# Optimization experiments

Hardware: AMD Instinct MI355X
Metric: run time of the kernel (lower is better)

## Reference

```python
import jax, jax.numpy as jnp
import numpy as np

B, S, D, H = 2, 2048, 1024, 16
HEAD_DIM = D // H  # 64


def setup_inputs() -> dict:
    key = jax.random.key(0)
    ks = jax.random.split(key, 7)
    x = jax.random.normal(ks[0], (B, S, D), dtype=jnp.float32)
    W_q = jax.random.normal(ks[1], (D, D), dtype=jnp.float32) * 0.02
    W_k = jax.random.normal(ks[2], (D, D), dtype=jnp.float32) * 0.02
    W_v = jax.random.normal(ks[3], (D, D), dtype=jnp.float32) * 0.02
    W_o = jax.random.normal(ks[4], (D, D), dtype=jnp.float32) * 0.02 / np.sqrt(2 * 12)
    b_o = jnp.zeros((D,), dtype=jnp.float32)
    # Ragged prefix attention_mask: per-row valid lengths in [S/2, S];
    # row 0 forced to full length so max_valid_len == S statically (jit-safe).
    lengths = jax.random.randint(ks[5], (B,), S // 2, S + 1)
    lengths = lengths.at[0].set(S)
    attention_mask = (jnp.arange(S)[None, :] < lengths[:, None]).astype(jnp.float32)
    return {"x": x, "attention_mask": attention_mask, "W_q": W_q, "W_k": W_k,
            "W_v": W_v, "W_o": W_o, "b_o": b_o}


def reference(x, attention_mask, W_q, W_k, W_v, W_o, b_o):
    b, s, d = x.shape
    h, hd = H, HEAD_DIM
    # QKV projections (no bias, qkv_bias=False)
    q = (x @ W_q.T).reshape(b, s, h, hd).transpose(0, 2, 1, 3)  # [b,h,s,hd]
    # Masking keys/values at invalid (padded) positions; for prefix masks this
    # is exactly the module's per-batch packing loop (max_valid_len == s).
    m = attention_mask[:, None, :, None]  # [b,1,s,1]
    k = ((x @ W_k.T).reshape(b, s, h, hd).transpose(0, 2, 1, 3)) * m
    v = ((x @ W_v.T).reshape(b, s, h, hd).transpose(0, 2, 1, 3)) * m
    # Naive causal attention, same op order as the torch module:
    # mask with -inf first, then scale by 1/sqrt(head_dim), then softmax.
    causal = jnp.triu(jnp.ones((s, s), dtype=bool), 1)  # True above diagonal
    scores = jnp.einsum('bhqd,bhkd->bhqk', q, k)
    scores = jnp.where(causal[None, None], -jnp.inf, scores)
    att = jax.nn.softmax(scores / jnp.sqrt(jnp.float32(hd)), axis=-1)
    ctx = jnp.einsum('bhqk,bhkd->bhqd', att, v)  # [b,h,s,hd]
    ctx = ctx.transpose(0, 2, 1, 3).reshape(b, s, d)
    # Output projection (dropout is inference no-op)
    return ctx @ W_o.T + b_o
```

## Files before the change

### kernel.cpp

```cpp
#include <hip/hip_runtime.h>

#define B_  2
#define S_  2048
#define D_  1024
#define H_  16
#define HD_ 64
#define N3_ 3072
#define M_  4096

typedef _Float16 f16;
typedef _Float16 f16x4 __attribute__((ext_vector_type(4)));
typedef _Float16 f16x8 __attribute__((ext_vector_type(8)));
typedef float    f32x4 __attribute__((ext_vector_type(4)));

__device__ __forceinline__ void async16(const f16* g, f16* l) {
  __builtin_amdgcn_global_load_lds(
      (const __attribute__((address_space(1))) unsigned int*)g,
      (__attribute__((address_space(3))) unsigned int*)l, 16, 0, 0);
}

__global__ __launch_bounds__(256)
void cvt_f32_f16(const float* __restrict__ src, f16* __restrict__ dst,
                 int n4, float scale) {
  int i = blockIdx.x * 256 + threadIdx.x;
  if (i >= n4) return;
  float4 v = ((const float4*)src)[i];
  f16x4 o = { (f16)(v.x * scale), (f16)(v.y * scale),
              (f16)(v.z * scale), (f16)(v.w * scale) };
  ((f16x4*)dst)[i] = o;
}

template<int QKV>
__global__ __launch_bounds__(256)
void gemm_nt(const f16* __restrict__ A, const f16* __restrict__ Bw,
             f16* __restrict__ Cq, float* __restrict__ Cf,
             const float* __restrict__ mask, const float* __restrict__ bias,
             int Ndim, int Kdim) {
  __shared__ f16 As[128 * 32];
  __shared__ f16 Bs[128 * 32];

  const int tid  = threadIdx.x;
  const int lane = tid & 63;
  const int w    = tid >> 6;
  const int lcol = lane & 15;
  const int quad = lane >> 4;
  const int wave_m = w >> 1, wave_n = w & 1;

  const int m0 = blockIdx.y * 128;
  const int n0 = blockIdx.x * 128;

  const int c  = (lane & 3) ^ ((lane >> 3) & 3);
  const int rr = lane >> 2;
  const int u0 = 2 * w, u1 = 2 * w + 1;
  const f16* gA0 = A  + (size_t)(m0 + u0 * 16 + rr) * Kdim + c * 8;
  const f16* gA1 = A  + (size_t)(m0 + u1 * 16 + rr) * Kdim + c * 8;
  const f16* gB0 = Bw + (size_t)(n0 + u0 * 16 + rr) * Kdim + c * 8;
  const f16* gB1 = Bw + (size_t)(n0 + u1 * 16 + rr) * Kdim + c * 8;
  f16* lA0 = As + u0 * 512;
  f16* lA1 = As + u1 * 512;
  f16* lB0 = Bs + u0 * 512;
  f16* lB1 = Bs + u1 * 512;

  int offA[4], offB[4];
#pragma unroll
  for (int i = 0; i < 4; i++) {
    int ra = wave_m * 64 + i * 16 + lcol;
    offA[i] = ra * 32 + ((quad ^ ((ra >> 1) & 3)) * 8);
    int rb = wave_n * 64 + i * 16 + lcol;
    offB[i] = rb * 32 + ((quad ^ ((rb >> 1) & 3)) * 8);
  }

  const f32x4 zero = {0.f, 0.f, 0.f, 0.f};
  f32x4 acc[4][4];
#pragma unroll
  for (int i = 0; i < 4; i++)
#pragma unroll
    for (int j = 0; j < 4; j++) acc[i][j] = zero;

  for (int k0 = 0; k0 < Kdim; k0 += 32) {
    __syncthreads();
    async16(gA0 + k0, lA0);
    async16(gA1 + k0, lA1);
    async16(gB0 + k0, lB0);
    async16(gB1 + k0, lB1);
    __syncthreads();

    f16x8 af[4], bf[4];
#pragma unroll
    for (int i = 0; i < 4; i++) af[i] = *(const f16x8*)(As + offA[i]);
#pragma unroll
    for (int i = 0; i < 4; i++) bf[i] = *(const f16x8*)(Bs + offB[i]);
#pragma unroll
    for (int mi = 0; mi < 4; mi++)
#pragma unroll
      for (int ni = 0; ni < 4; ni++)
        acc[mi][ni] = __builtin_amdgcn_mfma_f32_16x16x32_f16(
            af[mi], bf[ni], acc[mi][ni], 0, 0, 0);
  }

#pragma unroll
  for (int mi = 0; mi < 4; mi++) {
#pragma unroll
    for (int r = 0; r < 4; r++) {
      int mg = m0 + wave_m * 64 + mi * 16 + quad * 4 + r;
      float mk = QKV ? mask[mg] : 0.f;
#pragma unroll
      for (int ni = 0; ni < 4; ni++) {
        int ng = n0 + wave_n * 64 + ni * 16 + lcol;
        float v = acc[mi][ni][r];
        if (QKV) {
          if (ng >= D_) v *= mk;
          Cq[(size_t)mg * Ndim + ng] = (f16)v;
        } else {
          Cf[(size_t)mg * Ndim + ng] = v + bias[ng];
        }
      }
    }
  }
}

__global__ __launch_bounds__(256)
void transpose_v(const f16* __restrict__ qkv, f16* __restrict__ vt) {
  __shared__ f16 t[64][72];
  const int tid = threadIdx.x;
  const int bh  = blockIdx.y;
  const int b   = bh >> 4, h = bh & 15;
  const int s0  = blockIdx.x * 64;
  {
    const int hdc = (tid & 15) * 4;
    const int sl  = tid >> 4;
#pragma unroll
    for (int i = 0; i < 4; i++) {
      int s = sl + i * 16;
      f16x4 v = *(const f16x4*)(qkv + (size_t)(b * S_ + s0 + s) * N3_ +
                                2 * D_ + h * HD_ + hdc);
      *(f16x4*)&t[s][hdc] = v;
    }
  }
  __syncthreads();
  {
    const int sc4 = (tid & 15) * 4;
    const int hd  = tid >> 4;
#pragma unroll
    for (int i = 0; i < 4; i++) {
      int hh = hd + i * 16;
      f16x4 v = { t[sc4][hh], t[sc4 + 1][hh], t[sc4 + 2][hh], t[sc4 + 3][hh] };
      *(f16x4*)(vt + (size_t)(bh * HD_ + hh) * S_ + s0 + sc4) = v;
    }
  }
}

__global__ __launch_bounds__(256)
void flash_attn2(const f16* __restrict__ qkv, const f16* __restrict__ vt,
                 f16* __restrict__ ctx) {
  __shared__ f16 Ks[64 * 64];
  __shared__ f16 Vs[64 * 64];

  const int tid  = threadIdx.x;
  const int lane = tid & 63;
  const int w    = tid >> 6;
  const int lcol = lane & 15;
  const int quad = lane >> 4;
  const int lx   = lcol & 7;
  const int bh   = blockIdx.y;
  const int b    = bh >> 4, h = bh & 15;
  const int pair = blockIdx.x;

  const int rsub = lane >> 3;
  const int gch  = (lane & 7) ^ rsub;
  const int krow0 = w * 8 + rsub;
  const int krow1 = 32 + w * 8 + rsub;
  const f16* Kg = qkv + (size_t)b * S_ * N3_ + D_ + h * HD_;
  const f16* Vg = vt + (size_t)bh * HD_ * S_;
  f16* ldsK0 = Ks + (w * 8) * 64;
  f16* ldsK1 = Ks + (32 + w * 8) * 64;
  f16* ldsV0 = Vs + (w * 8) * 64;
  f16* ldsV1 = Vs + (32 + w * 8) * 64;

  const f32x4 zero = {0.f, 0.f, 0.f, 0.f};

  for (int phase = 0; phase < 2; phase++) {
    const int qt   = phase ? (31 - pair) : pair;
    const int qrow = qt * 64 + w * 16 + lcol;
    const f16* Qp = qkv + (size_t)(b * S_ + qrow) * N3_ + h * HD_;
    const f16x8 qb0 = *(const f16x8*)(Qp + quad * 8);
    const f16x8 qb1 = *(const f16x8*)(Qp + 32 + quad * 8);

    f32x4 o[4];
#pragma unroll
    for (int i = 0; i < 4; i++) o[i] = zero;
    float mx = -1e30f, lp = 0.f;

    for (int kt = 0; kt <= qt; kt++) {
      const int kbase = kt * 64;
      __syncthreads();
      async16(Kg + (size_t)(kbase + krow0) * N3_ + gch * 8, ldsK0);
      async16(Kg + (size_t)(kbase + krow1) * N3_ + gch * 8, ldsK1);
      async16(Vg + (size_t)krow0 * S_ + kbase + gch * 8, ldsV0);
      async16(Vg + (size_t)krow1 * S_ + kbase + gch * 8, ldsV1);
      __syncthreads();

      f32x4 sc[4];
#pragma unroll
      for (int ct = 0; ct < 4; ct++) {
        const f16* kr = Ks + (ct * 16 + lcol) * 64;
        f16x8 k0 = *(const f16x8*)(kr + ((quad    ) ^ lx) * 8);
        f16x8 k1 = *(const f16x8*)(kr + ((quad + 4) ^ lx) * 8);
        f32x4 z = zero;
        z = __builtin_amdgcn_mfma_f32_16x16x32_f16(k0, qb0, z, 0, 0, 0);
        z = __builtin_amdgcn_mfma_f32_16x16x32_f16(k1, qb1, z, 0, 0, 0);
        sc[ct] = z;
      }
      if (kt == qt) {
#pragma unroll
        for (int ct = 0; ct < 4; ct++) {
          int koff = ct * 16 + quad * 4;
          int qoff = w * 16 + lcol;
#pragma unroll
          for (int r = 0; r < 4; r++)
            if (koff + r > qoff) sc[ct][r] = -1e30f;
        }
      }
      float t = sc[0][0];
#pragma unroll
      for (int ct = 0; ct < 4; ct++)
#pragma unroll
        for (int r = 0; r < 4; r++) t = fmaxf(t, sc[ct][r]);
      t = fmaxf(t, __shfl_xor(t, 16));
      t = fmaxf(t, __shfl_xor(t, 32));
      const float nm = fmaxf(mx, t);
      const float alpha = exp2f(mx - nm);
      mx = nm;
      lp *= alpha;
#pragma unroll
      for (int ht = 0; ht < 4; ht++) {
#pragma unroll
        for (int r = 0; r < 4; r++) o[ht][r] *= alpha;
      }
      f16x4 pf[4];
#pragma unroll
      for (int ct = 0; ct < 4; ct++) {
        float e0 = exp2f(sc[ct][0] - nm);
        float e1 = exp2f(sc[ct][1] - nm);
        float e2 = exp2f(sc[ct][2] - nm);
        float e3 = exp2f(sc[ct][3] - nm);
        lp += (e0 + e1) + (e2 + e3);
        f16x4 p = { (f16)e0, (f16)e1, (f16)e2, (f16)e3 };
        pf[ct] = p;
      }
#pragma unroll
      for (int ht = 0; ht < 4; ht++) {
        const f16* vr = Vs + (ht * 16 + lcol) * 64 + (quad & 1) * 4;
#pragma unroll
        for (int ct = 0; ct < 4; ct++) {
          f16x4 vf = *(const f16x4*)(vr + (((2 * ct + (quad >> 1)) ^ lx) * 8));
          o[ht] = __builtin_amdgcn_mfma_f32_16x16x16f16(vf, pf[ct], o[ht], 0, 0, 0);
        }
      }
    }

    lp += __shfl_xor(lp, 16);
    lp += __shfl_xor(lp, 32);
    const float inv = 1.f / lp;
    f16* cp = ctx + (size_t)(b * S_ + qrow) * D_ + h * HD_ + quad * 4;
#pragma unroll
    for (int ht = 0; ht < 4; ht++) {
      f16x4 ov = { (f16)(o[ht][0] * inv), (f16)(o[ht][1] * inv),
                   (f16)(o[ht][2] * inv), (f16)(o[ht][3] * inv) };
      *(f16x4*)(cp + ht * 16) = ov;
    }
  }
}

extern "C" void kernel_launch(void* const* d_in, const int* in_sizes, int n_in,
                              void* d_out, int out_size, void* d_ws, size_t ws_size,
                              hipStream_t stream) {
  (void)in_sizes; (void)n_in; (void)out_size; (void)ws_size;
  const float* x  = (const float*)d_in[0];
  const float* am = (const float*)d_in[1];
  const float* Wq = (const float*)d_in[2];
  const float* Wk = (const float*)d_in[3];
  const float* Wv = (const float*)d_in[4];
  const float* Wo = (const float*)d_in[5];
  const float* bo = (const float*)d_in[6];
  float* out = (float*)d_out;

  f16* ws   = (f16*)d_ws;
  f16* wqkv = ws;
  f16* wo16 = wqkv + (size_t)3 * D_ * D_;
  f16* xb   = wo16 + (size_t)D_ * D_;
  f16* qkvb = xb + (size_t)M_ * D_;
  f16* vtb  = qkvb + (size_t)M_ * N3_;
  f16* ctxb = vtb + (size_t)M_ * D_;

  const float qscale = 0.125f * 1.4426950408889634f;

  cvt_f32_f16<<<dim3(M_ * D_ / 1024), 256, 0, stream>>>(x, xb, M_ * D_ / 4, 1.0f);
  cvt_f32_f16<<<dim3(D_ * D_ / 1024), 256, 0, stream>>>(Wq, wqkv, D_ * D_ / 4, qscale);
  cvt_f32_f16<<<dim3(D_ * D_ / 1024), 256, 0, stream>>>(Wk, wqkv + (size_t)D_ * D_, D_ * D_ / 4, 1.0f);
  cvt_f32_f16<<<dim3(D_ * D_ / 1024), 256, 0, stream>>>(Wv, wqkv + (size_t)2 * D_ * D_, D_ * D_ / 4, 1.0f);
  cvt_f32_f16<<<dim3(D_ * D_ / 1024), 256, 0, stream>>>(Wo, wo16, D_ * D_ / 4, 1.0f);

  gemm_nt<1><<<dim3(N3_ / 128, M_ / 128), 256, 0, stream>>>(
      xb, wqkv, qkvb, nullptr, am, nullptr, N3_, D_);
  transpose_v<<<dim3(S_ / 64, B_ * H_), 256, 0, stream>>>(qkvb, vtb);
  flash_attn2<<<dim3(16, B_ * H_), 256, 0, stream>>>(qkvb, vtb, ctxb);
  gemm_nt<0><<<dim3(D_ / 128, M_ / 128), 256, 0, stream>>>(
      ctxb, wo16, nullptr, out, nullptr, bo, D_, D_);
}
```

Baseline: 214.4 us.

## Share K/V tiles across paired query tiles, widen GEMM K-step, fuse weight casts

The flash attention kernel now walks both query tiles of a causal pair in one pass over keys, so each K/V tile is loaded once and reused for both. Previously the two tiles were processed one after the other, each reloading K/V. The block index is also remapped to a flat 1D grid that interleaves heads. Separately, the GEMM's K tile grows from 32 to 64 with a new XOR swizzle, halving the number of barrier pairs, and the four weight conversion launches are merged into one 2D launch. Costs are more registers for two accumulator sets and doubled LDS in the GEMM, which may lower occupancy.

```diff
diff --git a/kernel.cpp b/kernel.cpp
--- a/kernel.cpp
+++ b/kernel.cpp
@@ -30,44 +30,62 @@
   ((f16x4*)dst)[i] = o;
 }
 
+__global__ __launch_bounds__(256)
+void cvt_weights(const float* __restrict__ Wq, const float* __restrict__ Wk,
+                 const float* __restrict__ Wv, const float* __restrict__ Wo,
+                 f16* __restrict__ dst, float qscale) {
+  const int m = blockIdx.y;
+  const float* src = (m == 0) ? Wq : (m == 1) ? Wk : (m == 2) ? Wv : Wo;
+  const float scale = (m == 0) ? qscale : 1.0f;
+  int i = blockIdx.x * 256 + threadIdx.x;
+  float4 v = ((const float4*)src)[i];
+  f16x4 o = { (f16)(v.x * scale), (f16)(v.y * scale),
+              (f16)(v.z * scale), (f16)(v.w * scale) };
+  ((f16x4*)(dst + (size_t)m * D_ * D_))[i] = o;
+}
+
 template<int QKV>
 __global__ __launch_bounds__(256)
 void gemm_nt(const f16* __restrict__ A, const f16* __restrict__ Bw,
              f16* __restrict__ Cq, float* __restrict__ Cf,
              const float* __restrict__ mask, const float* __restrict__ bias,
              int Ndim, int Kdim) {
-  __shared__ f16 As[128 * 32];
-  __shared__ f16 Bs[128 * 32];
+  __shared__ f16 As[128 * 64];
+  __shared__ f16 Bs[128 * 64];
 
   const int tid  = threadIdx.x;
   const int lane = tid & 63;
   const int w    = tid >> 6;
   const int lcol = lane & 15;
   const int quad = lane >> 4;
+  const int lx   = lcol & 7;
   const int wave_m = w >> 1, wave_n = w & 1;
 
   const int m0 = blockIdx.y * 128;
   const int n0 = blockIdx.x * 128;
 
-  const int c  = (lane & 3) ^ ((lane >> 3) & 3);
-  const int rr = lane >> 2;
-  const int u0 = 2 * w, u1 = 2 * w + 1;
-  const f16* gA0 = A  + (size_t)(m0 + u0 * 16 + rr) * Kdim + c * 8;
-  const f16* gA1 = A  + (size_t)(m0 + u1 * 16 + rr) * Kdim + c * 8;
-  const f16* gB0 = Bw + (size_t)(n0 + u0 * 16 + rr) * Kdim + c * 8;
-  const f16* gB1 = Bw + (size_t)(n0 + u1 * 16 + rr) * Kdim + c * 8;
-  f16* lA0 = As + u0 * 512;
-  f16* lA1 = As + u1 * 512;
-  f16* lB0 = Bs + u0 * 512;
-  f16* lB1 = Bs + u1 * 512;
+  const int rr  = lane >> 3;
+  const int gch = (lane & 7) ^ rr;
+
+  const f16* gA[4];
+  const f16* gB[4];
+  f16* lA[4];
+  f16* lB[4];
+#pragma unroll
+  for (int i = 0; i < 4; i++) {
+    int seg = i * 4 + w;
+    int row = seg * 8 + rr;
+    gA[i] = A  + (size_t)(m0 + row) * Kdim + gch * 8;
+    gB[i] = Bw + (size_t)(n0 + row) * Kdim + gch * 8;
+    lA[i] = As + seg * 512;
+    lB[i] = Bs + seg * 512;
+  }
 
   int offA[4], offB[4];
 #pragma unroll
   for (int i = 0; i < 4; i++) {
-    int ra = wave_m * 64 + i * 16 + lcol;
-    offA[i] = ra * 32 + ((quad ^ ((ra >> 1) & 3)) * 8);
-    int rb = wave_n * 64 + i * 16 + lcol;
-    offB[i] = rb * 32 + ((quad ^ ((rb >> 1) & 3)) * 8);
+    offA[i] = (wave_m * 64 + i * 16 + lcol) * 64;
+    offB[i] = (wave_n * 64 + i * 16 + lcol) * 64;
   }
 
   const f32x4 zero = {0.f, 0.f, 0.f, 0.f};
@@ -77,25 +95,29 @@
 #pragma unroll
     for (int j = 0; j < 4; j++) acc[i][j] = zero;
 
-  for (int k0 = 0; k0 < Kdim; k0 += 32) {
+  for (int k0 = 0; k0 < Kdim; k0 += 64) {
     __syncthreads();
-    async16(gA0 + k0, lA0);
-    async16(gA1 + k0, lA1);
-    async16(gB0 + k0, lB0);
-    async16(gB1 + k0, lB1);
+#pragma unroll
+    for (int i = 0; i < 4; i++) async16(gA[i] + k0, lA[i]);
+#pragma unroll
+    for (int i = 0; i < 4; i++) async16(gB[i] + k0, lB[i]);
     __syncthreads();
 
-    f16x8 af[4], bf[4];
-#pragma unroll
-    for (int i = 0; i < 4; i++) af[i] = *(const f16x8*)(As + offA[i]);
-#pragma unroll
-    for (int i = 0; i < 4; i++) bf[i] = *(const f16x8*)(Bs + offB[i]);
-#pragma unroll
-    for (int mi = 0; mi < 4; mi++)
-#pragma unroll
-      for (int ni = 0; ni < 4; ni++)
-        acc[mi][ni] = __builtin_amdgcn_mfma_f32_16x16x32_f16(
-            af[mi], bf[ni], acc[mi][ni], 0, 0, 0);
+#pragma unroll
+    for (int ks = 0; ks < 2; ks++) {
+      const int co = ((quad + 4 * ks) ^ lx) * 8;
+      f16x8 af[4], bf[4];
+#pragma unroll
+      for (int i = 0; i < 4; i++) af[i] = *(const f16x8*)(As + offA[i] + co);
+#pragma unroll
+      for (int i = 0; i < 4; i++) bf[i] = *(const f16x8*)(Bs + offB[i] + co);
+#pragma unroll
+      for (int mi = 0; mi < 4; mi++)
+#pragma unroll
+        for (int ni = 0; ni < 4; ni++)
+          acc[mi][ni] = __builtin_amdgcn_mfma_f32_16x16x32_f16(
+              af[mi], bf[ni], acc[mi][ni], 0, 0, 0);
+    }
   }
 
 #pragma unroll
@@ -151,7 +173,7 @@
 }
 
 __global__ __launch_bounds__(256)
-void flash_attn2(const f16* __restrict__ qkv, const f16* __restrict__ vt,
+void flash_attn3(const f16* __restrict__ qkv, const f16* __restrict__ vt,
                  f16* __restrict__ ctx) {
   __shared__ f16 Ks[64 * 64];
   __shared__ f16 Vs[64 * 64];
@@ -162,9 +184,13 @@
   const int lcol = lane & 15;
   const int quad = lane >> 4;
   const int lx   = lcol & 7;
-  const int bh   = blockIdx.y;
+
+  const int id   = blockIdx.x;
+  const int bh   = (id & 7) + 8 * ((id >> 3) & 3);
+  const int pair = id >> 5;
   const int b    = bh >> 4, h = bh & 15;
-  const int pair = blockIdx.x;
+  const int qtA  = 31 - pair;
+  const int qtB  = pair;
 
   const int rsub = lane >> 3;
   const int gch  = (lane & 7) ^ rsub;
@@ -179,96 +205,110 @@
 
   const f32x4 zero = {0.f, 0.f, 0.f, 0.f};
 
-  for (int phase = 0; phase < 2; phase++) {
-    const int qt   = phase ? (31 - pair) : pair;
-    const int qrow = qt * 64 + w * 16 + lcol;
-    const f16* Qp = qkv + (size_t)(b * S_ + qrow) * N3_ + h * HD_;
-    const f16x8 qb0 = *(const f16x8*)(Qp + quad * 8);
-    const f16x8 qb1 = *(const f16x8*)(Qp + 32 + quad * 8);
-
-    f32x4 o[4];
-#pragma unroll
-    for (int i = 0; i < 4; i++) o[i] = zero;
-    float mx = -1e30f, lp = 0.f;
-
-    for (int kt = 0; kt <= qt; kt++) {
-      const int kbase = kt * 64;
-      __syncthreads();
-      async16(Kg + (size_t)(kbase + krow0) * N3_ + gch * 8, ldsK0);
-      async16(Kg + (size_t)(kbase + krow1) * N3_ + gch * 8, ldsK1);
-      async16(Vg + (size_t)krow0 * S_ + kbase + gch * 8, ldsV0);
-      async16(Vg + (size_t)krow1 * S_ + kbase + gch * 8, ldsV1);
-      __syncthreads();
-
-      f32x4 sc[4];
+  const int qrowA = qtA * 64 + w * 16 + lcol;
+  const int qrowB = qtB * 64 + w * 16 + lcol;
+  const f16* QpA = qkv + (size_t)(b * S_ + qrowA) * N3_ + h * HD_;
+  const f16* QpB = qkv + (size_t)(b * S_ + qrowB) * N3_ + h * HD_;
+  const f16x8 qbA0 = *(const f16x8*)(QpA + quad * 8);
+  const f16x8 qbA1 = *(const f16x8*)(QpA + 32 + quad * 8);
+  const f16x8 qbB0 = *(const f16x8*)(QpB + quad * 8);
+  const f16x8 qbB1 = *(const f16x8*)(QpB + 32 + quad * 8);
+
+  f32x4 oA[4], oB[4];
+  float mxA = -1e30f, lpA = 0.f, mxB = -1e30f, lpB = 0.f;
+#pragma unroll
+  for (int i = 0; i < 4; i++) { oA[i] = zero; oB[i] = zero; }
+
+  auto process = [&](int qt, const f16x8& qb0, const f16x8& qb1,
+                     f32x4* o, float& mx, float& lp, int kt) {
+    f32x4 sc[4];
+#pragma unroll
+    for (int ct = 0; ct < 4; ct++) {
+      const f16* kr = Ks + (ct * 16 + lcol) * 64;
+      f16x8 k0 = *(const f16x8*)(kr + ((quad    ) ^ lx) * 8);
+      f16x8 k1 = *(const f16x8*)(kr + ((quad + 4) ^ lx) * 8);
+      f32x4 z = zero;
+      z = __builtin_amdgcn_mfma_f32_16x16x32_f16(k0, qb0, z, 0, 0, 0);
+      z = __builtin_amdgcn_mfma_f32_16x16x32_f16(k1, qb1, z, 0, 0, 0);
+      sc[ct] = z;
+    }
+    if (kt == qt) {
 #pragma unroll
       for (int ct = 0; ct < 4; ct++) {
-        const f16* kr = Ks + (ct * 16 + lcol) * 64;
-        f16x8 k0 = *(const f16x8*)(kr + ((quad    ) ^ lx) * 8);
-        f16x8 k1 = *(const f16x8*)(kr + ((quad + 4) ^ lx) * 8);
-        f32x4 z = zero;
-        z = __builtin_amdgcn_mfma_f32_16x16x32_f16(k0, qb0, z, 0, 0, 0);
-        z = __builtin_amdgcn_mfma_f32_16x16x32_f16(k1, qb1, z, 0, 0, 0);
-        sc[ct] = z;
+        int koff = ct * 16 + quad * 4;
+        int qoff = w * 16 + lcol;
+#pragma unroll
+        for (int r = 0; r < 4; r++)
+          if (koff + r > qoff) sc[ct][r] = -1e30f;
       }
-      if (kt == qt) {
-#pragma unroll
-        for (int ct = 0; ct < 4; ct++) {
-          int koff = ct * 16 + quad * 4;
-          int qoff = w * 16 + lcol;
-#pragma unroll
-          for (int r = 0; r < 4; r++)
-            if (koff + r > qoff) sc[ct][r] = -1e30f;
-        }
+    }
+    float t = sc[0][0];
+#pragma unroll
+    for (int ct = 0; ct < 4; ct++)
+#pragma unroll
+      for (int r = 0; r < 4; r++) t = fmaxf(t, sc[ct][r]);
+    t = fmaxf(t, __shfl_xor(t, 16));
+    t = fmaxf(t, __shfl_xor(t, 32));
+    const float nm = fmaxf(mx, t);
+    const float alpha = exp2f(mx - nm);
+    mx = nm;
+    lp *= alpha;
+#pragma unroll
+    for (int ht = 0; ht < 4; ht++)
+#pragma unroll
+      for (int r = 0; r < 4; r++) o[ht][r] *= alpha;
+    f16x4 pf[4];
+#pragma unroll
+    for (int ct = 0; ct < 4; ct++) {
+      float e0 = exp2f(sc[ct][0] - nm);
+      float e1 = exp2f(sc[ct][1] - nm);
+      float e2 = exp2f(sc[ct][2] - nm);
+      float e3 = exp2f(sc[ct][3] - nm);
+      lp += (e0 + e1) + (e2 + e3);
+      f16x4 p = { (f16)e0, (f16)e1, (f16)e2, (f16)e3 };
+      pf[ct] = p;
+    }
+#pragma unroll
+    for (int ht = 0; ht < 4; ht++) {
+      const f16* vr = Vs + (ht * 16 + lcol) * 64 + (quad & 1) * 4;
+#pragma unroll
+      for (int ct = 0; ct < 4; ct++) {
+        f16x4 vf = *(const f16x4*)(vr + (((2 * ct + (quad >> 1)) ^ lx) * 8));
+        o[ht] = __builtin_amdgcn_mfma_f32_16x16x16f16(vf, pf[ct], o[ht], 0, 0, 0);
       }
-      float t = sc[0][0];
-#pragma unroll
-      for (int ct = 0; ct < 4; ct++)
-#pragma unroll
-        for (int r = 0; r < 4; r++) t = fmaxf(t, sc[ct][r]);
-      t = fmaxf(t, __shfl_xor(t, 16));
-      t = fmaxf(t, __shfl_xor(t, 32));
-      const float nm = fmaxf(mx, t);
-      const float alpha = exp2f(mx - nm);
-      mx = nm;
-      lp *= alpha;
-#pragma unroll
-      for (int ht = 0; ht < 4; ht++) {
-#pragma unroll
-        for (int r = 0; r < 4; r++) o[ht][r] *= alpha;
-      }
-      f16x4 pf[4];
-#pragma unroll
-      for (int ct = 0; ct < 4; ct++) {
-        float e0 = exp2f(sc[ct][0] - nm);
-        float e1 = exp2f(sc[ct][1] - nm);
-        float e2 = exp2f(sc[ct][2] - nm);
-        float e3 = exp2f(sc[ct][3] - nm);
-        lp += (e0 + e1) + (e2 + e3);
-        f16x4 p = { (f16)e0, (f16)e1, (f16)e2, (f16)e3 };
-        pf[ct] = p;
-      }
-#pragma unroll
-      for (int ht = 0; ht < 4; ht++) {
-        const f16* vr = Vs + (ht * 16 + lcol) * 64 + (quad & 1) * 4;
-#pragma unroll
-        for (int ct = 0; ct < 4; ct++) {
-          f16x4 vf = *(const f16x4*)(vr + (((2 * ct + (quad >> 1)) ^ lx) * 8));
-          o[ht] = __builtin_amdgcn_mfma_f32_16x16x16f16(vf, pf[ct], o[ht], 0, 0, 0);
-        }
-      }
-    }
-
-    lp += __shfl_xor(lp, 16);
-    lp += __shfl_xor(lp, 32);
-    const float inv = 1.f / lp;
-    f16* cp = ctx + (size_t)(b * S_ + qrow) * D_ + h * HD_ + quad * 4;
-#pragma unroll
-    for (int ht = 0; ht < 4; ht++) {
-      f16x4 ov = { (f16)(o[ht][0] * inv), (f16)(o[ht][1] * inv),
-                   (f16)(o[ht][2] * inv), (f16)(o[ht][3] * inv) };
-      *(f16x4*)(cp + ht * 16) = ov;
-    }
+    }
+  };
+
+  for (int kt = 0; kt <= qtA; kt++) {
+    const int kbase = kt * 64;
+    __syncthreads();
+    async16(Kg + (size_t)(kbase + krow0) * N3_ + gch * 8, ldsK0);
+    async16(Kg + (size_t)(kbase + krow1) * N3_ + gch * 8, ldsK1);
+    async16(Vg + (size_t)krow0 * S_ + kbase + gch * 8, ldsV0);
+    async16(Vg + (size_t)krow1 * S_ + kbase + gch * 8, ldsV1);
+    __syncthreads();
+
+    process(qtA, qbA0, qbA1, oA, mxA, lpA, kt);
+    if (kt <= qtB)
+      process(qtB, qbB0, qbB1, oB, mxB, lpB, kt);
+  }
+
+  lpA += __shfl_xor(lpA, 16);
+  lpA += __shfl_xor(lpA, 32);
+  lpB += __shfl_xor(lpB, 16);
+  lpB += __shfl_xor(lpB, 32);
+  const float invA = 1.f / lpA;
+  const float invB = 1.f / lpB;
+  f16* cpA = ctx + (size_t)(b * S_ + qrowA) * D_ + h * HD_ + quad * 4;
+  f16* cpB = ctx + (size_t)(b * S_ + qrowB) * D_ + h * HD_ + quad * 4;
+#pragma unroll
+  for (int ht = 0; ht < 4; ht++) {
+    f16x4 ovA = { (f16)(oA[ht][0] * invA), (f16)(oA[ht][1] * invA),
+                  (f16)(oA[ht][2] * invA), (f16)(oA[ht][3] * invA) };
+    *(f16x4*)(cpA + ht * 16) = ovA;
+    f16x4 ovB = { (f16)(oB[ht][0] * invB), (f16)(oB[ht][1] * invB),
+                  (f16)(oB[ht][2] * invB), (f16)(oB[ht][3] * invB) };
+    *(f16x4*)(cpB + ht * 16) = ovB;
   }
 }
 
@@ -296,15 +336,12 @@
   const float qscale = 0.125f * 1.4426950408889634f;
 
   cvt_f32_f16<<<dim3(M_ * D_ / 1024), 256, 0, stream>>>(x, xb, M_ * D_ / 4, 1.0f);
-  cvt_f32_f16<<<dim3(D_ * D_ / 1024), 256, 0, stream>>>(Wq, wqkv, D_ * D_ / 4, qscale);
-  cvt_f32_f16<<<dim3(D_ * D_ / 1024), 256, 0, stream>>>(Wk, wqkv + (size_t)D_ * D_, D_ * D_ / 4, 1.0f);
-  cvt_f32_f16<<<dim3(D_ * D_ / 1024), 256, 0, stream>>>(Wv, wqkv + (size_t)2 * D_ * D_, D_ * D_ / 4, 1.0f);
-  cvt_f32_f16<<<dim3(D_ * D_ / 1024), 256, 0, stream>>>(Wo, wo16, D_ * D_ / 4, 1.0f);
+  cvt_weights<<<dim3(D_ * D_ / 1024, 4), 256, 0, stream>>>(Wq, Wk, Wv, Wo, wqkv, qscale);
 
   gemm_nt<1><<<dim3(N3_ / 128, M_ / 128), 256, 0, stream>>>(
       xb, wqkv, qkvb, nullptr, am, nullptr, N3_, D_);
   transpose_v<<<dim3(S_ / 64, B_ * H_), 256, 0, stream>>>(qkvb, vtb);
-  flash_attn2<<<dim3(16, B_ * H_), 256, 0, stream>>>(qkvb, vtb, ctxb);
+  flash_attn3<<<dim3(512), 256, 0, stream>>>(qkvb, vtb, ctxb);
   gemm_nt<0><<<dim3(D_ / 128, M_ / 128), 256, 0, stream>>>(
       ctxb, wo16, nullptr, out, nullptr, bo, D_, D_);
 }
```

Result: faster. 207.3 us (-3.3%).
